# Kernel tuning notes

Hardware: AMD Instinct MI355X
Metric: run time of the kernel (lower is better)

The kernel has to match this reference:

```python
import jax, jax.numpy as jnp
import numpy as np

D_MODEL = 1024
H = 16
D_K = D_MODEL // H
B, S = 4, 2048


def setup_inputs() -> dict:
    key = jax.random.key(0)
    ks = jax.random.split(key, 12)
    s = 1.0 / np.sqrt(D_MODEL)
    inp = {
        "q": jax.random.normal(ks[0], (B, S, D_MODEL), jnp.float32),
        "k": jax.random.normal(ks[1], (B, S, D_MODEL), jnp.float32),
        "v": jax.random.normal(ks[2], (B, S, D_MODEL), jnp.float32),
        "mask": jax.random.randint(ks[3], (1, 1, S, S), 0, 2, jnp.int32),
        # torch nn.Linear convention: weight [out, in], y = x @ W.T + b
        "w_q": jax.random.uniform(ks[4], (D_MODEL, D_MODEL), jnp.float32, -s, s),
        "b_q": jax.random.uniform(ks[5], (D_MODEL,), jnp.float32, -s, s),
        "w_k": jax.random.uniform(ks[6], (D_MODEL, D_MODEL), jnp.float32, -s, s),
        "b_k": jax.random.uniform(ks[7], (D_MODEL,), jnp.float32, -s, s),
        "w_v": jax.random.uniform(ks[8], (D_MODEL, D_MODEL), jnp.float32, -s, s),
        "b_v": jax.random.uniform(ks[9], (D_MODEL,), jnp.float32, -s, s),
        "w_o": jax.random.uniform(ks[10], (D_MODEL, D_MODEL), jnp.float32, -s, s),
        "b_o": jax.random.uniform(ks[11], (D_MODEL,), jnp.float32, -s, s),
    }
    return inp


def _split_heads(x):
    b, s, _ = x.shape
    return x.reshape(b, s, H, D_K).transpose(0, 2, 1, 3)  # [B,H,S,Dk]


def reference(q, k, v, mask, w_q, b_q, w_k, b_k, w_v, b_v, w_o, b_o):
    query = _split_heads(q @ w_q.T + b_q)
    key = _split_heads(k @ w_k.T + b_k)
    value = _split_heads(v @ w_v.T + b_v)
    scores = jnp.einsum("bhqd,bhkd->bhqk", query, key) / jnp.sqrt(
        jnp.asarray(D_K, query.dtype))
    scores = jnp.where(mask == 0, jnp.asarray(-1e9, scores.dtype), scores)
    attn = jax.nn.softmax(scores, axis=-1)  # dropout p=0 (eval) -> identity
    x = jnp.einsum("bhqk,bhkd->bhqd", attn, value)
    x = x.transpose(0, 2, 1, 3).reshape(q.shape[0], -1, H * D_K)
    return x @ w_o.T + b_o
```

## Files before the change

kernel.cpp:

```cpp
#include <hip/hip_runtime.h>

typedef __bf16 bf16_t;
typedef __bf16 bf16x4 __attribute__((ext_vector_type(4)));
typedef __bf16 bf16x8 __attribute__((ext_vector_type(8)));
typedef float f32x4 __attribute__((ext_vector_type(4)));
typedef float f32x16 __attribute__((ext_vector_type(16)));
typedef unsigned int uint;
typedef uint uint4v __attribute__((ext_vector_type(4)));

static __device__ __forceinline__ bf16_t f2bf(float f) {
  unsigned u = __builtin_bit_cast(unsigned, f);
  u = (u + 0x7fff + ((u >> 16) & 1)) >> 16;
  unsigned short h = (unsigned short)u;
  return __builtin_bit_cast(bf16_t, h);
}
static __device__ __forceinline__ uint pack2(float a, float b) {
  uint lo = __builtin_bit_cast(unsigned short, (bf16_t)a);
  uint hi = __builtin_bit_cast(unsigned short, (bf16_t)b);
  return lo | (hi << 16);
}

__global__ void cvt_f2b(const float* __restrict__ in, bf16_t* __restrict__ out, int n4) {
  int i = blockIdx.x * blockDim.x + threadIdx.x;
  if (i >= n4) return;
  const float4 f = reinterpret_cast<const float4*>(in)[i];
  bf16x4 o;
  o[0] = f2bf(f.x); o[1] = f2bf(f.y); o[2] = f2bf(f.z); o[3] = f2bf(f.w);
  reinterpret_cast<bf16x4*>(out)[i] = o;
}

__global__ void mask_bits_k(const int* __restrict__ m, uint* __restrict__ out) {
  int i = blockIdx.x * 256 + threadIdx.x;
  int q = i & 2047, t = i >> 11;
  const int* mrow = m + (size_t)q * 2048 + t * 32;
  uint bits = 0;
#pragma unroll
  for (int j = 0; j < 16; ++j) {
    int r0 = (j & 3) + 8 * (j >> 2);
    bits |= (mrow[r0] ? 1u : 0u) << j;
    bits |= (mrow[r0 + 4] ? 1u : 0u) << (16 + j);
  }
  out[(size_t)t * 2048 + q] = bits;
}

#define GLD_LDS(g, l) \
  __builtin_amdgcn_global_load_lds((const __attribute__((address_space(1))) void*)(g), \
                                   (__attribute__((address_space(3))) void*)(l), 16, 0, 0)

template <int OM>
__global__ __launch_bounds__(256, 2) void gemm_bias(
    const bf16_t* __restrict__ A, const bf16_t* __restrict__ Bw,
    const float* __restrict__ bias, void* __restrict__ Cout) {
  constexpr int K = 1024, N = 1024;
  __shared__ bf16_t As[128 * 32];
  __shared__ bf16_t Bs[128 * 32];
  const int tid = threadIdx.x;
  const int lane = tid & 63;
  const int wave = tid >> 6;
  const int wm = (wave >> 1) * 64, wn = (wave & 1) * 64;
  const int l15 = lane & 15, lhi = lane >> 4;
  const int bm = blockIdx.x, bn = blockIdx.y;
  const int r0 = tid >> 2;
  const int kc = (tid & 3) * 8;
  const bf16_t* ga = A + (size_t)(bm * 128 + r0) * K + kc;
  const bf16_t* gb = Bw + (size_t)(bn * 128 + r0) * K + kc;
  char* ldsA = (char*)As + wave * 1024;
  char* ldsB = (char*)Bs + wave * 1024;
  f32x4 acc[4][4] = {};
  for (int k0 = 0; k0 < K; k0 += 32) {
    __syncthreads();
    GLD_LDS(ga + k0, ldsA);
    GLD_LDS(ga + 64 * K + k0, ldsA + 4096);
    GLD_LDS(gb + k0, ldsB);
    GLD_LDS(gb + 64 * K + k0, ldsB + 4096);
    __syncthreads();
    bf16x8 af[4], bfv[4];
#pragma unroll
    for (int i = 0; i < 4; ++i)
      af[i] = *reinterpret_cast<const bf16x8*>(&As[(wm + i * 16 + l15) * 32 + lhi * 8]);
#pragma unroll
    for (int j = 0; j < 4; ++j)
      bfv[j] = *reinterpret_cast<const bf16x8*>(&Bs[(wn + j * 16 + l15) * 32 + lhi * 8]);
#pragma unroll
    for (int i = 0; i < 4; ++i)
#pragma unroll
      for (int j = 0; j < 4; ++j)
        acc[i][j] = __builtin_amdgcn_mfma_f32_16x16x32_bf16(af[i], bfv[j], acc[i][j], 0, 0, 0);
  }
#pragma unroll
  for (int i = 0; i < 4; ++i) {
#pragma unroll
    for (int j = 0; j < 4; ++j) {
      int n = bn * 128 + wn + j * 16 + l15;
      float bv = bias[n];
#pragma unroll
      for (int r = 0; r < 4; ++r) {
        int m = bm * 128 + wm + i * 16 + lhi * 4 + r;
        float val = acc[i][j][r] + bv;
        if (OM == 0) {
          ((bf16_t*)Cout)[(size_t)m * N + n] = f2bf(val);
        } else if (OM == 1) {
          int b = m >> 11, s = m & 2047;
          ((bf16_t*)Cout)[((size_t)b * 1024 + n) * 2048 + s] = f2bf(val);
        } else {
          ((float*)Cout)[(size_t)m * N + n] = val;
        }
      }
    }
  }
}

__global__ __launch_bounds__(256, 4) void attn_kernel(
    const bf16_t* __restrict__ Qp, const bf16_t* __restrict__ Kp,
    const bf16_t* __restrict__ Vt, const uint* __restrict__ maskbits,
    bf16_t* __restrict__ Xb) {
  constexpr int S = 2048, D = 1024;
  constexpr float CS = 0.18033688011112042f;
  __shared__ __align__(16) bf16_t Ks[2][32][72];
  __shared__ __align__(16) bf16_t Vs[2][64][40];
  const int tid = threadIdx.x;
  const int wave = tid >> 6, lane = tid & 63;
  const int l31 = lane & 31, h = lane >> 5;
  const int blk = blockIdx.x;
  const int bh = blk & 63, qt4 = blk >> 6;
  const int b = bh >> 4, hd = bh & 15;
  const int q0 = qt4 * 128 + wave * 32;

  const int rK = tid >> 3, sK = tid & 7;
  const int rV = tid >> 2, sV = tid & 3;
  const bf16_t* gK = Kp + (size_t)b * S * D + (size_t)rK * D + hd * 64 + sK * 8;
  const bf16_t* gV = Vt + ((size_t)b * 1024 + hd * 64 + rV) * (size_t)S + sV * 8;

  const bf16_t* qbase = Qp + (size_t)(b * S + q0 + l31) * D + hd * 64 + h * 8;
  bf16x8 qf[4];
#pragma unroll
  for (int c = 0; c < 4; ++c)
    qf[c] = *reinterpret_cast<const bf16x8*>(qbase + 16 * c);

  const uint* mbase = maskbits + q0 + l31;

  f32x16 o0 = {}, o1 = {};
  float mrun = 0.f, lsum = 0.f;

  {
    bf16x8 k0r = *reinterpret_cast<const bf16x8*>(gK);
    bf16x8 v0r = *reinterpret_cast<const bf16x8*>(gV);
    *reinterpret_cast<bf16x8*>(&Ks[0][rK][sK * 8]) = k0r;
    *reinterpret_cast<bf16x8*>(&Vs[0][rV][sV * 8]) = v0r;
    __syncthreads();
  }

#pragma unroll 2
  for (int t = 0; t < 64; ++t) {
    const int cur = t & 1, nxt = cur ^ 1;
    const bool pf = (t < 63);
    bf16x8 kreg, vreg;
    if (pf) {
      kreg = *reinterpret_cast<const bf16x8*>(gK + (size_t)(t + 1) * 32 * D);
      vreg = *reinterpret_cast<const bf16x8*>(gV + (t + 1) * 32);
    }
    uint mbc = mbase[t * 2048];
    f32x16 s = {};
    __builtin_amdgcn_s_setprio(1);
#pragma unroll
    for (int c = 0; c < 4; ++c) {
      bf16x8 kf = *reinterpret_cast<const bf16x8*>(&Ks[cur][l31][h * 8 + 16 * c]);
      s = __builtin_amdgcn_mfma_f32_32x32x16_bf16(kf, qf[c], s, 0, 0, 0);
    }
    __builtin_amdgcn_s_setprio(0);
    const uint mbh = mbc >> (h << 4);
    float x0 = fmaxf(s[0], s[1]), x1 = fmaxf(s[2], s[3]);
    float x2 = fmaxf(s[4], s[5]), x3 = fmaxf(s[6], s[7]);
    float x4 = fmaxf(s[8], s[9]), x5 = fmaxf(s[10], s[11]);
    float x6 = fmaxf(s[12], s[13]), x7 = fmaxf(s[14], s[15]);
    x0 = fmaxf(x0, x1); x2 = fmaxf(x2, x3); x4 = fmaxf(x4, x5); x6 = fmaxf(x6, x7);
    x0 = fmaxf(x0, x2); x4 = fmaxf(x4, x6);
    float mt = fmaxf(x0, x4);
    mt = fmaxf(mt, __shfl_xor(mt, 32));
    if (!__all(mt - mrun <= 44.36142f)) {
      float mnew = fmaxf(mrun, mt);
      float alpha = __builtin_amdgcn_exp2f((mrun - mnew) * CS);
#pragma unroll
      for (int r = 0; r < 16; ++r) { o0[r] *= alpha; o1[r] *= alpha; }
      lsum *= alpha;
      mrun = mnew;
    }
    const float mc = mrun * CS;
    float p[16];
#pragma unroll
    for (int r = 0; r < 16; ++r) {
      float pv = __builtin_amdgcn_exp2f(__builtin_fmaf(s[r], CS, -mc));
      uint smask = (uint)(((int)(mbh << (31 - r))) >> 31);
      p[r] = __builtin_bit_cast(float, __builtin_bit_cast(uint, pv) & smask);
    }
    float t0 = p[0] + p[1], t1 = p[2] + p[3], t2 = p[4] + p[5], t3 = p[6] + p[7];
    float t4 = p[8] + p[9], t5 = p[10] + p[11], t6 = p[12] + p[13], t7 = p[14] + p[15];
    t0 += t1; t2 += t3; t4 += t5; t6 += t7;
    t0 += t2; t4 += t6;
    float ts = t0 + t4;
    ts += __shfl_xor(ts, 32);
    lsum += ts;
    uint dw[8];
#pragma unroll
    for (int i = 0; i < 8; ++i) dw[i] = pack2(p[2 * i], p[2 * i + 1]);
    uint e0 = (uint)__shfl_xor((int)(h ? dw[0] : dw[2]), 32);
    uint e1 = (uint)__shfl_xor((int)(h ? dw[1] : dw[3]), 32);
    uint e2 = (uint)__shfl_xor((int)(h ? dw[4] : dw[6]), 32);
    uint e3 = (uint)__shfl_xor((int)(h ? dw[5] : dw[7]), 32);
    uint4v ua0 = {h ? e0 : dw[0], h ? e1 : dw[1], h ? dw[2] : e0, h ? dw[3] : e1};
    uint4v ua1 = {h ? e2 : dw[4], h ? e3 : dw[5], h ? dw[6] : e2, h ? dw[7] : e3};
    bf16x8 pa0 = __builtin_bit_cast(bf16x8, ua0);
    bf16x8 pa1 = __builtin_bit_cast(bf16x8, ua1);
    {
      bf16x8 v00 = *reinterpret_cast<const bf16x8*>(&Vs[cur][l31][h * 8]);
      bf16x8 v01 = *reinterpret_cast<const bf16x8*>(&Vs[cur][l31][16 + h * 8]);
      bf16x8 v10 = *reinterpret_cast<const bf16x8*>(&Vs[cur][32 + l31][h * 8]);
      bf16x8 v11 = *reinterpret_cast<const bf16x8*>(&Vs[cur][32 + l31][16 + h * 8]);
      __builtin_amdgcn_s_setprio(1);
      o0 = __builtin_amdgcn_mfma_f32_32x32x16_bf16(pa0, v00, o0, 0, 0, 0);
      o0 = __builtin_amdgcn_mfma_f32_32x32x16_bf16(pa1, v01, o0, 0, 0, 0);
      o1 = __builtin_amdgcn_mfma_f32_32x32x16_bf16(pa0, v10, o1, 0, 0, 0);
      o1 = __builtin_amdgcn_mfma_f32_32x32x16_bf16(pa1, v11, o1, 0, 0, 0);
      __builtin_amdgcn_s_setprio(0);
    }
    if (pf) {
      *reinterpret_cast<bf16x8*>(&Ks[nxt][rK][sK * 8]) = kreg;
      *reinterpret_cast<bf16x8*>(&Vs[nxt][rV][sV * 8]) = vreg;
      __syncthreads();
    }
  }
  float linv = 1.f / lsum;
  bf16_t* xrow = Xb + (size_t)(b * S + q0) * D + hd * 64 + l31;
#pragma unroll
  for (int r = 0; r < 16; ++r) {
    int qrow = (r & 3) + 8 * (r >> 2) + 4 * h;
    float lr = __shfl(linv, qrow);
    xrow[(size_t)qrow * D] = f2bf(o0[r] * lr);
    xrow[(size_t)qrow * D + 32] = f2bf(o1[r] * lr);
  }
}

extern "C" void kernel_launch(void* const* d_in, const int* in_sizes, int n_in,
                              void* d_out, int out_size, void* d_ws, size_t ws_size,
                              hipStream_t stream) {
  const float* q = (const float*)d_in[0];
  const float* k = (const float*)d_in[1];
  const float* v = (const float*)d_in[2];
  const int* mask = (const int*)d_in[3];
  const float* w_q = (const float*)d_in[4];
  const float* b_q = (const float*)d_in[5];
  const float* w_k = (const float*)d_in[6];
  const float* b_k = (const float*)d_in[7];
  const float* w_v = (const float*)d_in[8];
  const float* b_v = (const float*)d_in[9];
  const float* w_o = (const float*)d_in[10];
  const float* b_o = (const float*)d_in[11];

  char* ws = (char*)d_ws;
  const size_t SZ = (size_t)8192 * 1024 * 2;
  bf16_t* qc = (bf16_t*)(ws + 0 * SZ);
  bf16_t* kc = (bf16_t*)(ws + 1 * SZ);
  bf16_t* vc = (bf16_t*)(ws + 2 * SZ);
  bf16_t* Qp = (bf16_t*)(ws + 3 * SZ);
  bf16_t* Kp = (bf16_t*)(ws + 4 * SZ);
  bf16_t* Vt = (bf16_t*)(ws + 5 * SZ);
  bf16_t* Xb = (bf16_t*)(ws + 6 * SZ);
  uint* maskB = (uint*)(ws + 7 * SZ);
  bf16_t* wqb = (bf16_t*)(ws + 7 * SZ + 8388608);
  bf16_t* wkb = wqb + 1048576;
  bf16_t* wvb = wkb + 1048576;
  bf16_t* wob = wvb + 1048576;

  cvt_f2b<<<8192, 256, 0, stream>>>(q, qc, 2097152);
  cvt_f2b<<<8192, 256, 0, stream>>>(k, kc, 2097152);
  cvt_f2b<<<8192, 256, 0, stream>>>(v, vc, 2097152);
  cvt_f2b<<<1024, 256, 0, stream>>>(w_q, wqb, 262144);
  cvt_f2b<<<1024, 256, 0, stream>>>(w_k, wkb, 262144);
  cvt_f2b<<<1024, 256, 0, stream>>>(w_v, wvb, 262144);
  cvt_f2b<<<1024, 256, 0, stream>>>(w_o, wob, 262144);
  mask_bits_k<<<512, 256, 0, stream>>>(mask, maskB);

  dim3 gg(64, 8);
  gemm_bias<0><<<gg, 256, 0, stream>>>(qc, wqb, b_q, Qp);
  gemm_bias<0><<<gg, 256, 0, stream>>>(kc, wkb, b_k, Kp);
  gemm_bias<1><<<gg, 256, 0, stream>>>(vc, wvb, b_v, Vt);
  attn_kernel<<<1024, 256, 0, stream>>>(Qp, Kp, Vt, maskB, Xb);
  gemm_bias<2><<<gg, 256, 0, stream>>>(Xb, wob, b_o, d_out);
}
```

Baseline: 268.7 us.

## Merge conversion launches and compute softmax row sums with MFMA

The seven fp32-to-bf16 conversion launches are merged into two kernels (activations and weights), which removes launch overhead. In the attention loop, the per-tile scalar sum of probabilities and its cross-lane shuffle are replaced by two extra MFMAs against a ones vector that accumulate the row sum in matrix layout, so no shuffle is needed at the end. The change also uses the hardware packed bf16 convert, a bitfield-extract for the mask, and a reshaped max tree. In exchange it adds MFMA work per tile, holds 16 more accumulator registers, and sums the bf16-rounded probabilities rather than the fp32 ones.

```diff
diff --git a/kernel.cpp b/kernel.cpp
--- a/kernel.cpp
+++ b/kernel.cpp
@@ -14,19 +14,42 @@
   unsigned short h = (unsigned short)u;
   return __builtin_bit_cast(bf16_t, h);
 }
-static __device__ __forceinline__ uint pack2(float a, float b) {
-  uint lo = __builtin_bit_cast(unsigned short, (bf16_t)a);
-  uint hi = __builtin_bit_cast(unsigned short, (bf16_t)b);
-  return lo | (hi << 16);
-}
-
-__global__ void cvt_f2b(const float* __restrict__ in, bf16_t* __restrict__ out, int n4) {
-  int i = blockIdx.x * blockDim.x + threadIdx.x;
-  if (i >= n4) return;
-  const float4 f = reinterpret_cast<const float4*>(in)[i];
+static __device__ __forceinline__ uint cvt_pk(float a, float b) {
+  uint r;
+  asm("v_cvt_pk_bf16_f32 %0, %1, %2" : "=v"(r) : "v"(a), "v"(b));
+  return r;
+}
+
+__global__ void cvt3_f2b(const float* __restrict__ a, const float* __restrict__ b,
+                         const float* __restrict__ c, bf16_t* __restrict__ oa,
+                         bf16_t* __restrict__ ob, bf16_t* __restrict__ oc) {
+  int i = blockIdx.x * 256 + threadIdx.x;
+  const float* src = a;
+  bf16_t* dst = oa;
+  if (i >= 4194304) { src = c; dst = oc; i -= 4194304; }
+  else if (i >= 2097152) { src = b; dst = ob; i -= 2097152; }
+  const float4 f = reinterpret_cast<const float4*>(src)[i];
   bf16x4 o;
   o[0] = f2bf(f.x); o[1] = f2bf(f.y); o[2] = f2bf(f.z); o[3] = f2bf(f.w);
-  reinterpret_cast<bf16x4*>(out)[i] = o;
+  reinterpret_cast<bf16x4*>(dst)[i] = o;
+}
+
+__global__ void cvt4_f2b(const float* __restrict__ a, const float* __restrict__ b,
+                         const float* __restrict__ c, const float* __restrict__ d,
+                         bf16_t* __restrict__ oa, bf16_t* __restrict__ ob,
+                         bf16_t* __restrict__ oc, bf16_t* __restrict__ od) {
+  int i = blockIdx.x * 256 + threadIdx.x;
+  const float* src = a;
+  bf16_t* dst = oa;
+  int w = i >> 18;
+  i &= 262143;
+  if (w == 1) { src = b; dst = ob; }
+  else if (w == 2) { src = c; dst = oc; }
+  else if (w == 3) { src = d; dst = od; }
+  const float4 f = reinterpret_cast<const float4*>(src)[i];
+  bf16x4 o;
+  o[0] = f2bf(f.x); o[1] = f2bf(f.y); o[2] = f2bf(f.z); o[3] = f2bf(f.w);
+  reinterpret_cast<bf16x4*>(dst)[i] = o;
 }
 
 __global__ void mask_bits_k(const int* __restrict__ m, uint* __restrict__ out) {
@@ -139,8 +162,12 @@
 
   const uint* mbase = maskbits + q0 + l31;
 
-  f32x16 o0 = {}, o1 = {};
-  float mrun = 0.f, lsum = 0.f;
+  bf16x8 ones;
+#pragma unroll
+  for (int i = 0; i < 8; ++i) ones[i] = (bf16_t)1.0f;
+
+  f32x16 o0 = {}, o1 = {}, osum = {};
+  float mrun = 0.f;
 
   {
     bf16x8 k0r = *reinterpret_cast<const bf16x8*>(gK);
@@ -169,20 +196,20 @@
     }
     __builtin_amdgcn_s_setprio(0);
     const uint mbh = mbc >> (h << 4);
-    float x0 = fmaxf(s[0], s[1]), x1 = fmaxf(s[2], s[3]);
-    float x2 = fmaxf(s[4], s[5]), x3 = fmaxf(s[6], s[7]);
-    float x4 = fmaxf(s[8], s[9]), x5 = fmaxf(s[10], s[11]);
-    float x6 = fmaxf(s[12], s[13]), x7 = fmaxf(s[14], s[15]);
-    x0 = fmaxf(x0, x1); x2 = fmaxf(x2, x3); x4 = fmaxf(x4, x5); x6 = fmaxf(x6, x7);
-    x0 = fmaxf(x0, x2); x4 = fmaxf(x4, x6);
-    float mt = fmaxf(x0, x4);
+    float a0 = fmaxf(fmaxf(s[0], s[1]), s[2]);
+    float a1 = fmaxf(fmaxf(s[3], s[4]), s[5]);
+    float a2 = fmaxf(fmaxf(s[6], s[7]), s[8]);
+    float a3 = fmaxf(fmaxf(s[9], s[10]), s[11]);
+    float a4 = fmaxf(fmaxf(s[12], s[13]), s[14]);
+    float b0 = fmaxf(fmaxf(a0, a1), a2);
+    float b1 = fmaxf(a3, a4);
+    float mt = fmaxf(fmaxf(b0, b1), s[15]);
     mt = fmaxf(mt, __shfl_xor(mt, 32));
     if (!__all(mt - mrun <= 44.36142f)) {
       float mnew = fmaxf(mrun, mt);
       float alpha = __builtin_amdgcn_exp2f((mrun - mnew) * CS);
 #pragma unroll
-      for (int r = 0; r < 16; ++r) { o0[r] *= alpha; o1[r] *= alpha; }
-      lsum *= alpha;
+      for (int r = 0; r < 16; ++r) { o0[r] *= alpha; o1[r] *= alpha; osum[r] *= alpha; }
       mrun = mnew;
     }
     const float mc = mrun * CS;
@@ -190,19 +217,12 @@
 #pragma unroll
     for (int r = 0; r < 16; ++r) {
       float pv = __builtin_amdgcn_exp2f(__builtin_fmaf(s[r], CS, -mc));
-      uint smask = (uint)(((int)(mbh << (31 - r))) >> 31);
+      uint smask = (uint)__builtin_amdgcn_sbfe((int)mbh, r, 1);
       p[r] = __builtin_bit_cast(float, __builtin_bit_cast(uint, pv) & smask);
     }
-    float t0 = p[0] + p[1], t1 = p[2] + p[3], t2 = p[4] + p[5], t3 = p[6] + p[7];
-    float t4 = p[8] + p[9], t5 = p[10] + p[11], t6 = p[12] + p[13], t7 = p[14] + p[15];
-    t0 += t1; t2 += t3; t4 += t5; t6 += t7;
-    t0 += t2; t4 += t6;
-    float ts = t0 + t4;
-    ts += __shfl_xor(ts, 32);
-    lsum += ts;
     uint dw[8];
 #pragma unroll
-    for (int i = 0; i < 8; ++i) dw[i] = pack2(p[2 * i], p[2 * i + 1]);
+    for (int i = 0; i < 8; ++i) dw[i] = cvt_pk(p[2 * i], p[2 * i + 1]);
     uint e0 = (uint)__shfl_xor((int)(h ? dw[0] : dw[2]), 32);
     uint e1 = (uint)__shfl_xor((int)(h ? dw[1] : dw[3]), 32);
     uint e2 = (uint)__shfl_xor((int)(h ? dw[4] : dw[6]), 32);
@@ -221,6 +241,8 @@
       o0 = __builtin_amdgcn_mfma_f32_32x32x16_bf16(pa1, v01, o0, 0, 0, 0);
       o1 = __builtin_amdgcn_mfma_f32_32x32x16_bf16(pa0, v10, o1, 0, 0, 0);
       o1 = __builtin_amdgcn_mfma_f32_32x32x16_bf16(pa1, v11, o1, 0, 0, 0);
+      osum = __builtin_amdgcn_mfma_f32_32x32x16_bf16(pa0, ones, osum, 0, 0, 0);
+      osum = __builtin_amdgcn_mfma_f32_32x32x16_bf16(pa1, ones, osum, 0, 0, 0);
       __builtin_amdgcn_s_setprio(0);
     }
     if (pf) {
@@ -229,12 +251,11 @@
       __syncthreads();
     }
   }
-  float linv = 1.f / lsum;
   bf16_t* xrow = Xb + (size_t)(b * S + q0) * D + hd * 64 + l31;
 #pragma unroll
   for (int r = 0; r < 16; ++r) {
     int qrow = (r & 3) + 8 * (r >> 2) + 4 * h;
-    float lr = __shfl(linv, qrow);
+    float lr = __builtin_amdgcn_rcpf(osum[r]);
     xrow[(size_t)qrow * D] = f2bf(o0[r] * lr);
     xrow[(size_t)qrow * D + 32] = f2bf(o1[r] * lr);
   }
@@ -271,13 +292,8 @@
   bf16_t* wvb = wkb + 1048576;
   bf16_t* wob = wvb + 1048576;
 
-  cvt_f2b<<<8192, 256, 0, stream>>>(q, qc, 2097152);
-  cvt_f2b<<<8192, 256, 0, stream>>>(k, kc, 2097152);
-  cvt_f2b<<<8192, 256, 0, stream>>>(v, vc, 2097152);
-  cvt_f2b<<<1024, 256, 0, stream>>>(w_q, wqb, 262144);
-  cvt_f2b<<<1024, 256, 0, stream>>>(w_k, wkb, 262144);
-  cvt_f2b<<<1024, 256, 0, stream>>>(w_v, wvb, 262144);
-  cvt_f2b<<<1024, 256, 0, stream>>>(w_o, wob, 262144);
+  cvt3_f2b<<<24576, 256, 0, stream>>>(q, k, v, qc, kc, vc);
+  cvt4_f2b<<<4096, 256, 0, stream>>>(w_q, w_k, w_v, w_o, wqb, wkb, wvb, wob);
   mask_bits_k<<<512, 256, 0, stream>>>(mask, maskB);
 
   dim3 gg(64, 8);
```

After: 249.3 us. 1.08x faster.
